# Performance work log

Measured on AMD Instinct MI355X. Metric: run time of the kernel, lower is better.

## Reference

```python
import jax, jax.numpy as jnp
import numpy as np

NUM_HEADS = 8
CHUNK = 64


def _retention(q, k, v):
    # q, k: (B, H, L, DK); v: (B, H, L, DV). Chunked linear retention with
    # per-head exponential decay gamma_h = 1 - 2^(-5-h) (RetNet convention).
    B, Hn, L, DK = q.shape
    DV = v.shape[-1]
    C = CHUNK
    N = L // C
    dt = q.dtype
    gamma = (1.0 - jnp.exp2(-5.0 - jnp.arange(Hn, dtype=jnp.float32))).astype(dt)  # (H,)
    q = q * (DK ** -0.5)
    idx = jnp.arange(C)
    diff = idx[:, None] - idx[None, :]
    # intra-chunk causal decay mask D[h,i,j] = gamma_h^(i-j) for i>=j else 0
    D = jnp.where(diff >= 0, gamma[:, None, None] ** diff, 0.0).astype(dt)      # (H,C,C)
    decay_q = (gamma[:, None] ** (idx[None, :] + 1)).astype(dt)                 # (H,C)
    decay_k = (gamma[:, None] ** (C - 1 - idx[None, :])).astype(dt)             # (H,C)
    decay_s = (gamma ** C).astype(dt)                                           # (H,)

    def to_chunks(x):
        return jnp.moveaxis(x.reshape(B, Hn, N, C, -1), 2, 0)  # (N,B,H,C,d)

    qs, ks, vs = map(to_chunks, (q, k, v))

    def step(S, x):
        qc, kc, vc = x  # (B,H,C,dk) / (B,H,C,dv)
        attn = jnp.einsum('bhid,bhjd->bhij', qc, kc) * D
        o_intra = jnp.einsum('bhij,bhje->bhie', attn, vc)
        o_inter = jnp.einsum('bhid,bhde->bhie', qc * decay_q[None, :, :, None], S)
        S_new = decay_s[None, :, None, None] * S + jnp.einsum(
            'bhjd,bhje->bhde', kc * decay_k[None, :, :, None], vc)
        return S_new, o_intra + o_inter

    S0 = jnp.zeros((B, Hn, DK, DV), dt)
    _, o = jax.lax.scan(step, S0, (qs, ks, vs))  # (N,B,H,C,DV)
    return jnp.moveaxis(o, 0, 2).reshape(B, Hn, L, DV)


def _xavier(key, fan_in, fan_out, gain=2 ** (-2.5)):
    limit = gain * np.sqrt(6.0 / (fan_in + fan_out))
    return jax.random.uniform(key, (fan_in, fan_out), jnp.float32, -limit, limit)


def setup_inputs() -> dict:
    key = jax.random.key(0)
    k0, k1, k2, k3, k4 = jax.random.split(key, 5)
    B, L, D = 2, 4096, 1024
    return {
        'hidden_states': jax.random.normal(k0, (B, L, D), jnp.float32),
        'rel_pos': jnp.zeros((1,), jnp.float32),  # unused by the module's forward
        'Wq': _xavier(k1, D, D),
        'Wk': _xavier(k2, D, D),
        'Wv': _xavier(k3, D, D),
        'Wo': _xavier(k4, D, D),
    }


def reference(hidden_states, rel_pos, Wq, Wk, Wv, Wo):
    B, L, Dm = hidden_states.shape
    Hd = Dm // NUM_HEADS
    q = (hidden_states @ Wq).reshape(B, L, NUM_HEADS, Hd).transpose(0, 2, 1, 3)
    k = (hidden_states @ Wk).reshape(B, L, NUM_HEADS, Hd).transpose(0, 2, 1, 3)
    v = (hidden_states @ Wv).reshape(B, L, NUM_HEADS, Hd).transpose(0, 2, 1, 3)
    o = _retention(q, k, v)  # (B,H,L,Hd)
    o = o.transpose(0, 2, 1, 3).reshape(B, L, Dm)
    return o @ Wo
```

## Files before the change

kernel.cpp:

```cpp
#include <hip/hip_runtime.h>
#include <hip/hip_bf16.h>

typedef __bf16 bf16;
typedef __bf16 bf16x8 __attribute__((ext_vector_type(8)));
typedef float f32x4 __attribute__((ext_vector_type(4)));

#define MFMA16(a, b, c) __builtin_amdgcn_mfma_f32_16x16x32_bf16((a), (b), (c), 0, 0, 0)


__device__ __forceinline__ void g2l16(const bf16* g, bf16* l) {
  __builtin_amdgcn_global_load_lds(
      (const __attribute__((address_space(1))) void*)g,
      (__attribute__((address_space(3))) void*)l, 16, 0, 0);
}

__global__ __launch_bounds__(256) void cvt_bf16(const float* __restrict__ X,
                                                bf16* __restrict__ Y) {
  const size_t i = ((size_t)blockIdx.x * 256 + threadIdx.x) * 8;
  float4 a = *(const float4*)&X[i];
  float4 b = *(const float4*)&X[i + 4];
  union { bf16 h[8]; uint4 u; } p;
  p.h[0] = (bf16)a.x; p.h[1] = (bf16)a.y; p.h[2] = (bf16)a.z; p.h[3] = (bf16)a.w;
  p.h[4] = (bf16)b.x; p.h[5] = (bf16)b.y; p.h[6] = (bf16)b.z; p.h[7] = (bf16)b.w;
  *(uint4*)&Y[i] = p.u;
}

__global__ __launch_bounds__(256) void transpose_w(
    const float* __restrict__ Wq, const float* __restrict__ Wk,
    const float* __restrict__ Wv, const float* __restrict__ Wo,
    bf16* __restrict__ Wt) {
  __shared__ bf16 t[64 * 72];
  const float* src = (blockIdx.z == 0) ? Wq : (blockIdx.z == 1) ? Wk
                     : (blockIdx.z == 2) ? Wv : Wo;
  bf16* dst = Wt + (size_t)blockIdx.z * 1024 * 1024;
  const int k0 = blockIdx.x * 64, n0 = blockIdx.y * 64;
  const int tid = threadIdx.x;
#pragma unroll
  for (int s = 0; s < 4; ++s) {
    int u = tid + s * 256;
    int r = u >> 4, c4 = (u & 15) * 4;
    float4 f = *(const float4*)&src[(size_t)(k0 + r) * 1024 + n0 + c4];
    t[r * 72 + c4 + 0] = (bf16)f.x;
    t[r * 72 + c4 + 1] = (bf16)f.y;
    t[r * 72 + c4 + 2] = (bf16)f.z;
    t[r * 72 + c4 + 3] = (bf16)f.w;
  }
  __syncthreads();
#pragma unroll
  for (int s = 0; s < 2; ++s) {
    int u = tid + s * 256;
    int r = u >> 3, cc = u & 7;
    union { bf16 h[8]; uint4 u4; } pk;
#pragma unroll
    for (int j = 0; j < 8; ++j) pk.h[j] = t[(cc * 8 + j) * 72 + r];
    *(uint4*)&dst[(size_t)(n0 + r) * 1024 + k0 + cc * 8] = pk.u4;
  }
}

template <typename TC, int QKV>
__global__ __launch_bounds__(256) void gemm_lds(
    const bf16* __restrict__ A, const bf16* __restrict__ Bt,
    TC* __restrict__ C, float alpha) {
  __shared__ bf16 lA[128 * 64];
  __shared__ bf16 lB[128 * 64];
  const int m0 = blockIdx.x * 128, n0 = blockIdx.y * 128;
  if (QKV) {
    Bt += (size_t)blockIdx.z * 1024 * 1024;
    C += (size_t)blockIdx.z * 8192 * 1024;
    if (blockIdx.z != 0) alpha = 1.0f;
  }
  const int tid = threadIdx.x;
  const int w = tid >> 6, lane = tid & 63, lr = lane & 15, quad = lane >> 4;
  const int wm = w >> 1, wn = w & 1;

  const int srow = w * 32 + (lane >> 3);
  const int clog = (lane & 7) ^ ((lane >> 3) & 7);
  const bf16* gA = A + (size_t)(m0 + srow) * 1024 + clog * 8;
  const bf16* gB = Bt + (size_t)(n0 + srow) * 1024 + clog * 8;

  f32x4 acc[4][4] = {};

  for (int it = 0; it < 16; ++it) {
    const int k0 = it * 64;
#pragma unroll
    for (int is = 0; is < 4; ++is) {
      g2l16(gA + (size_t)is * 8 * 1024 + k0, &lA[(w * 32 + is * 8) * 64]);
      g2l16(gB + (size_t)is * 8 * 1024 + k0, &lB[(w * 32 + is * 8) * 64]);
    }
    __syncthreads();
#pragma unroll
    for (int kk = 0; kk < 2; ++kk) {
      bf16x8 af[4], bfv[4];
#pragma unroll
      for (int i = 0; i < 4; ++i) {
        const int m = wm * 64 + i * 16 + lr;
        af[i] = *(bf16x8*)&lA[m * 64 + (((kk * 4 + quad) ^ (lr & 7)) * 8)];
      }
#pragma unroll
      for (int j = 0; j < 4; ++j) {
        const int n = wn * 64 + j * 16 + lr;
        bfv[j] = *(bf16x8*)&lB[n * 64 + (((kk * 4 + quad) ^ (lr & 7)) * 8)];
      }
#pragma unroll
      for (int i = 0; i < 4; ++i)
#pragma unroll
        for (int j = 0; j < 4; ++j)
          acc[i][j] = MFMA16(af[i], bfv[j], acc[i][j]);
    }
    __syncthreads();
  }
#pragma unroll
  for (int i = 0; i < 4; ++i) {
#pragma unroll
    for (int j = 0; j < 4; ++j) {
      const int row = m0 + wm * 64 + i * 16 + quad * 4;
      const int col = n0 + wn * 64 + j * 16 + lr;
#pragma unroll
      for (int r = 0; r < 4; ++r)
        C[(size_t)(row + r) * 1024 + col] = (TC)(acc[i][j][r] * alpha);
    }
  }
}

__global__ __launch_bounds__(256) void chunk_kv(
    const bf16* __restrict__ kb, const bf16* __restrict__ vb,
    bf16* __restrict__ Tb) {
  __shared__ bf16 lK[128 * 72];
  __shared__ bf16 lV[128 * 72];
  const int g = blockIdx.x;
  const int bh = g >> 6, n = g & 63, b = bh >> 3, h = bh & 7;
  const float log2g = log2f(1.0f - exp2f(-5.0f - (float)h));
  const int tid = threadIdx.x;
  const size_t rowbase = (size_t)(b * 4096 + n * 64) * 1024 + h * 128;
  const bf16* kc = kb + rowbase;
  const bf16* vc = vb + rowbase;
#pragma unroll
  for (int s = 0; s < 4; ++s) {
    int u = tid + s * 256;
    int c = u >> 4, d0 = (u & 15) * 8;
    union { uint4 u4; bf16 h8[8]; } kv, vv;
    kv.u4 = *(const uint4*)&kc[(size_t)c * 1024 + d0];
    vv.u4 = *(const uint4*)&vc[(size_t)c * 1024 + d0];
    const float dec = exp2f((float)(63 - c) * log2g);
#pragma unroll
    for (int j = 0; j < 8; ++j) {
      lK[(d0 + j) * 72 + c] = (bf16)((float)kv.h8[j] * dec);
      lV[(d0 + j) * 72 + c] = vv.h8[j];
    }
  }
  __syncthreads();
  const int w = tid >> 6, lane = tid & 63, lr = lane & 15, quad = lane >> 4;
  const int wm = w >> 1, wn = w & 1;
  f32x4 acc[4][4] = {};
#pragma unroll
  for (int kk = 0; kk < 2; ++kk) {
    bf16x8 af[4], bv[4];
#pragma unroll
    for (int i = 0; i < 4; ++i)
      af[i] = *(bf16x8*)&lK[(wm * 64 + i * 16 + lr) * 72 + kk * 32 + quad * 8];
#pragma unroll
    for (int j = 0; j < 4; ++j)
      bv[j] = *(bf16x8*)&lV[(wn * 64 + j * 16 + lr) * 72 + kk * 32 + quad * 8];
#pragma unroll
    for (int i = 0; i < 4; ++i)
#pragma unroll
      for (int j = 0; j < 4; ++j)
        acc[i][j] = MFMA16(af[i], bv[j], acc[i][j]);
  }
  bf16* tchunk = Tb + (size_t)g * 16384;
#pragma unroll
  for (int i = 0; i < 4; ++i) {
#pragma unroll
    for (int j = 0; j < 4; ++j) {
      const int dk = wm * 64 + i * 16 + quad * 4;
      const int dv = wn * 64 + j * 16 + lr;
      union { bf16 h4[4]; uint2 u2; } pk;
#pragma unroll
      for (int r = 0; r < 4; ++r) pk.h4[r] = (bf16)acc[i][j][r];
      *(uint2*)&tchunk[(size_t)dv * 128 + dk] = pk.u2;
    }
  }
}

__global__ __launch_bounds__(256) void scan_state(bf16* __restrict__ Tb) {
  const int blk = blockIdx.x;
  const int bh = blk >> 6, seg = blk & 63, h = bh & 7;
  const float gs = exp2f(64.0f * log2f(1.0f - exp2f(-5.0f - (float)h)));
  const size_t base = (size_t)bh * 64 * 16384 + (size_t)seg * 256 + threadIdx.x;
  float S = 0.0f;
#pragma unroll 8
  for (int n = 0; n < 64; ++n) {
    const size_t a = base + (size_t)n * 16384;
    const float t = (float)Tb[a];
    Tb[a] = (bf16)S;
    S = gs * S + t;
  }
}

__global__ __launch_bounds__(256) void chunk_out(
    const bf16* __restrict__ qb, const bf16* __restrict__ kb,
    const bf16* __restrict__ vb, const bf16* __restrict__ Sp,
    bf16* __restrict__ ob) {
  __shared__ bf16 lQ[64 * 136];
  __shared__ bf16 lK[64 * 136];
  __shared__ bf16 lVt[128 * 72];
  __shared__ bf16 lP[64 * 72];
  const int g = blockIdx.x;
  const int bh = g >> 6, n = g & 63, b = bh >> 3, h = bh & 7;
  const float log2g = log2f(1.0f - exp2f(-5.0f - (float)h));
  const int tid = threadIdx.x;
  const size_t rowbase = (size_t)(b * 4096 + n * 64) * 1024 + h * 128;
  const bf16* qc = qb + rowbase;
  const bf16* kc = kb + rowbase;
  const bf16* vc = vb + rowbase;
#pragma unroll
  for (int s = 0; s < 4; ++s) {
    int u = tid + s * 256;
    int c = u >> 4, d0 = (u & 15) * 8;
    *(uint4*)&lQ[c * 136 + d0] = *(const uint4*)&qc[(size_t)c * 1024 + d0];
    *(uint4*)&lK[c * 136 + d0] = *(const uint4*)&kc[(size_t)c * 1024 + d0];
    union { uint4 u4; bf16 h8[8]; } vv;
    vv.u4 = *(const uint4*)&vc[(size_t)c * 1024 + d0];
#pragma unroll
    for (int j = 0; j < 8; ++j) lVt[(d0 + j) * 72 + c] = vv.h8[j];
  }
  __syncthreads();
  const int w = tid >> 6, lane = tid & 63, lr = lane & 15, quad = lane >> 4;

  f32x4 p[4] = {};
#pragma unroll
  for (int kk = 0; kk < 4; ++kk) {
    bf16x8 bfrag = *(bf16x8*)&lK[(w * 16 + lr) * 136 + kk * 32 + quad * 8];
#pragma unroll
    for (int i = 0; i < 4; ++i) {
      bf16x8 afrag = *(bf16x8*)&lQ[(i * 16 + lr) * 136 + kk * 32 + quad * 8];
      p[i] = MFMA16(afrag, bfrag, p[i]);
    }
  }
#pragma unroll
  for (int i = 0; i < 4; ++i) {
#pragma unroll
    for (int r = 0; r < 4; ++r) {
      const int row = i * 16 + quad * 4 + r;
      const int col = w * 16 + lr;
      const int diff = row - col;
      const float val =
          (diff >= 0) ? p[i][r] * exp2f((float)diff * log2g) : 0.0f;
      lP[row * 72 + col] = (bf16)val;
    }
  }
  __syncthreads();

  f32x4 oacc[4][2] = {};
#pragma unroll
  for (int j = 0; j < 2; ++j) {
    const int dvt = w * 32 + j * 16;
#pragma unroll
    for (int kk = 0; kk < 2; ++kk) {
      bf16x8 bfrag = *(bf16x8*)&lVt[(dvt + lr) * 72 + kk * 32 + quad * 8];
#pragma unroll
      for (int i = 0; i < 4; ++i) {
        bf16x8 afrag = *(bf16x8*)&lP[(i * 16 + lr) * 72 + kk * 32 + quad * 8];
        oacc[i][j] = MFMA16(afrag, bfrag, oacc[i][j]);
      }
    }
  }

  const bf16* sp = Sp + (size_t)g * 16384;
#pragma unroll
  for (int kk = 0; kk < 4; ++kk) {
    bf16x8 aN[4];
#pragma unroll
    for (int i = 0; i < 4; ++i) {
      bf16x8 a0 = *(bf16x8*)&lQ[(i * 16 + lr) * 136 + kk * 32 + quad * 8];
      const float dq = exp2f((float)(i * 16 + lr + 1) * log2g);
#pragma unroll
      for (int e = 0; e < 8; ++e) a0[e] = (bf16)((float)a0[e] * dq);
      aN[i] = a0;
    }
#pragma unroll
    for (int j = 0; j < 2; ++j) {
      bf16x8 bfrag =
          *(const bf16x8*)&sp[(size_t)(w * 32 + j * 16 + lr) * 128 + kk * 32 + quad * 8];
#pragma unroll
      for (int i = 0; i < 4; ++i) oacc[i][j] = MFMA16(aN[i], bfrag, oacc[i][j]);
    }
  }

  bf16* oc = ob + rowbase;
#pragma unroll
  for (int i = 0; i < 4; ++i)
#pragma unroll
    for (int j = 0; j < 2; ++j)
#pragma unroll
      for (int r = 0; r < 4; ++r) {
        const int row = i * 16 + quad * 4 + r;
        const int col = w * 32 + j * 16 + lr;
        oc[(size_t)row * 1024 + col] = (bf16)oacc[i][j][r];
      }
}

extern "C" void kernel_launch(void* const* d_in, const int* in_sizes, int n_in,
                              void* d_out, int out_size, void* d_ws,
                              size_t ws_size, hipStream_t stream) {
  const float* X  = (const float*)d_in[0];
  const float* Wq = (const float*)d_in[2];
  const float* Wk = (const float*)d_in[3];
  const float* Wv = (const float*)d_in[4];
  const float* Wo = (const float*)d_in[5];

  char* ws = (char*)d_ws;
  const size_t SZ_QKV = (size_t)8192 * 1024 * sizeof(bf16);
  bf16* qb = (bf16*)(ws);
  bf16* ob = (bf16*)(ws + 3 * SZ_QKV);
  bf16* Tb = (bf16*)(ws + 4 * SZ_QKV);
  bf16* Wt = (bf16*)(ws + 6 * SZ_QKV);
  bf16* Xb = (bf16*)(ws + 6 * SZ_QKV + (size_t)4 * 1024 * 1024 * sizeof(bf16));
  bf16* kb = qb + (size_t)8192 * 1024;
  bf16* vb = kb + (size_t)8192 * 1024;

  cvt_bf16<<<4096, 256, 0, stream>>>(X, Xb);
  transpose_w<<<dim3(16, 16, 4), 256, 0, stream>>>(Wq, Wk, Wv, Wo, Wt);

  const float qscale = 0.08838834764831845f;
  gemm_lds<bf16, 1><<<dim3(64, 8, 3), 256, 0, stream>>>(Xb, Wt, qb, qscale);

  chunk_kv<<<1024, 256, 0, stream>>>(kb, vb, Tb);
  scan_state<<<1024, 256, 0, stream>>>(Tb);
  chunk_out<<<1024, 256, 0, stream>>>(qb, kb, vb, Tb, ob);

  gemm_lds<float, 0><<<dim3(64, 8), 256, 0, stream>>>(
      ob, Wt + (size_t)3 * 1024 * 1024, (float*)d_out, 1.0f);
}
```

Before: 232.4 us.

## Emit chunk-transposed K/V from QKV GEMM and streamline retention kernels

```diff
diff --git a/kernel.cpp b/kernel.cpp
--- a/kernel.cpp
+++ b/kernel.cpp
@@ -14,27 +14,30 @@
       (__attribute__((address_space(3))) void*)l, 16, 0, 0);
 }
 
-__global__ __launch_bounds__(256) void cvt_bf16(const float* __restrict__ X,
-                                                bf16* __restrict__ Y) {
-  const size_t i = ((size_t)blockIdx.x * 256 + threadIdx.x) * 8;
-  float4 a = *(const float4*)&X[i];
-  float4 b = *(const float4*)&X[i + 4];
-  union { bf16 h[8]; uint4 u; } p;
-  p.h[0] = (bf16)a.x; p.h[1] = (bf16)a.y; p.h[2] = (bf16)a.z; p.h[3] = (bf16)a.w;
-  p.h[4] = (bf16)b.x; p.h[5] = (bf16)b.y; p.h[6] = (bf16)b.z; p.h[7] = (bf16)b.w;
-  *(uint4*)&Y[i] = p.u;
-}
-
-__global__ __launch_bounds__(256) void transpose_w(
-    const float* __restrict__ Wq, const float* __restrict__ Wk,
-    const float* __restrict__ Wv, const float* __restrict__ Wo,
-    bf16* __restrict__ Wt) {
+__global__ __launch_bounds__(256) void prep(
+    const float* __restrict__ X, const float* __restrict__ Wq,
+    const float* __restrict__ Wk, const float* __restrict__ Wv,
+    const float* __restrict__ Wo, bf16* __restrict__ Wt,
+    bf16* __restrict__ Xb) {
+  const int tid = threadIdx.x;
+  if (blockIdx.z == 4) {
+#pragma unroll
+    for (int it = 0; it < 16; ++it) {
+      const size_t i = (((size_t)blockIdx.x * 16 + it) * 256 + tid) * 8;
+      float4 a = *(const float4*)&X[i];
+      float4 b = *(const float4*)&X[i + 4];
+      union { bf16 h[8]; uint4 u; } p;
+      p.h[0] = (bf16)a.x; p.h[1] = (bf16)a.y; p.h[2] = (bf16)a.z; p.h[3] = (bf16)a.w;
+      p.h[4] = (bf16)b.x; p.h[5] = (bf16)b.y; p.h[6] = (bf16)b.z; p.h[7] = (bf16)b.w;
+      *(uint4*)&Xb[i] = p.u;
+    }
+    return;
+  }
   __shared__ bf16 t[64 * 72];
   const float* src = (blockIdx.z == 0) ? Wq : (blockIdx.z == 1) ? Wk
                      : (blockIdx.z == 2) ? Wv : Wo;
   bf16* dst = Wt + (size_t)blockIdx.z * 1024 * 1024;
-  const int k0 = blockIdx.x * 64, n0 = blockIdx.y * 64;
-  const int tid = threadIdx.x;
+  const int k0 = (blockIdx.x >> 4) * 64, n0 = (blockIdx.x & 15) * 64;
 #pragma unroll
   for (int s = 0; s < 4; ++s) {
     int u = tid + s * 256;
@@ -57,16 +60,16 @@
   }
 }
 
-template <typename TC, int QKV>
+template <typename TC, int MODE>
 __global__ __launch_bounds__(256) void gemm_lds(
     const bf16* __restrict__ A, const bf16* __restrict__ Bt,
-    TC* __restrict__ C, float alpha) {
+    TC* __restrict__ C, bf16* __restrict__ kTb, bf16* __restrict__ vTb,
+    float alpha) {
   __shared__ bf16 lA[128 * 64];
   __shared__ bf16 lB[128 * 64];
   const int m0 = blockIdx.x * 128, n0 = blockIdx.y * 128;
-  if (QKV) {
+  if (MODE) {
     Bt += (size_t)blockIdx.z * 1024 * 1024;
-    C += (size_t)blockIdx.z * 8192 * 1024;
     if (blockIdx.z != 0) alpha = 1.0f;
   }
   const int tid = threadIdx.x;
@@ -115,38 +118,54 @@
     for (int j = 0; j < 4; ++j) {
       const int row = m0 + wm * 64 + i * 16 + quad * 4;
       const int col = n0 + wn * 64 + j * 16 + lr;
-#pragma unroll
-      for (int r = 0; r < 4; ++r)
-        C[(size_t)(row + r) * 1024 + col] = (TC)(acc[i][j][r] * alpha);
+      if (MODE == 0 || blockIdx.z < 2) {
+        TC* Cz = C + (MODE ? (size_t)blockIdx.z * 8192 * 1024 : 0);
+#pragma unroll
+        for (int r = 0; r < 4; ++r)
+          Cz[(size_t)(row + r) * 1024 + col] = (TC)(acc[i][j][r] * alpha);
+      }
+      if (MODE == 1 && blockIdx.z >= 1) {
+        bf16* Tp = (blockIdx.z == 1) ? kTb : vTb;
+        const int b = row >> 12, pos = row & 4095;
+        const int n = pos >> 6, c0 = pos & 63;
+        const int h = col >> 7, d = col & 127;
+        union { bf16 h4[4]; uint2 u2; } pk;
+#pragma unroll
+        for (int r = 0; r < 4; ++r) pk.h4[r] = (bf16)acc[i][j][r];
+        *(uint2*)&Tp[((size_t)((b * 8 + h) * 64 + n)) * 8192 + d * 64 + c0] = pk.u2;
+      }
     }
   }
 }
 
 __global__ __launch_bounds__(256) void chunk_kv(
-    const bf16* __restrict__ kb, const bf16* __restrict__ vb,
+    const bf16* __restrict__ kT, const bf16* __restrict__ vT,
     bf16* __restrict__ Tb) {
-  __shared__ bf16 lK[128 * 72];
-  __shared__ bf16 lV[128 * 72];
+  __shared__ bf16 lK[128 * 64];
+  __shared__ bf16 lV[128 * 64];
   const int g = blockIdx.x;
-  const int bh = g >> 6, n = g & 63, b = bh >> 3, h = bh & 7;
-  const float log2g = log2f(1.0f - exp2f(-5.0f - (float)h));
+  const int h = (g >> 6) & 7;
+  const float lg = log2f(1.0f - exp2f(-5.0f - (float)h));
+  const float ginv = exp2f(-lg);
   const int tid = threadIdx.x;
-  const size_t rowbase = (size_t)(b * 4096 + n * 64) * 1024 + h * 128;
-  const bf16* kc = kb + rowbase;
-  const bf16* vc = vb + rowbase;
+  const bf16* ks = kT + (size_t)g * 8192;
+  const bf16* vs = vT + (size_t)g * 8192;
 #pragma unroll
   for (int s = 0; s < 4; ++s) {
     int u = tid + s * 256;
-    int c = u >> 4, d0 = (u & 15) * 8;
-    union { uint4 u4; bf16 h8[8]; } kv, vv;
-    kv.u4 = *(const uint4*)&kc[(size_t)c * 1024 + d0];
-    vv.u4 = *(const uint4*)&vc[(size_t)c * 1024 + d0];
-    const float dec = exp2f((float)(63 - c) * log2g);
-#pragma unroll
-    for (int j = 0; j < 8; ++j) {
-      lK[(d0 + j) * 72 + c] = (bf16)((float)kv.h8[j] * dec);
-      lV[(d0 + j) * 72 + c] = vv.h8[j];
-    }
+    int d = u >> 3, c0 = (u & 7) * 8;
+    int pc = ((u & 7) ^ (d & 7)) * 8;
+    *(uint4*)&lV[d * 64 + pc] = *(const uint4*)&vs[d * 64 + c0];
+    union { uint4 u4; bf16 h8[8]; } kv;
+    kv.u4 = *(const uint4*)&ks[d * 64 + c0];
+    float e = exp2f((float)(63 - c0) * lg);
+    union { bf16 h8[8]; uint4 u4; } o;
+#pragma unroll
+    for (int jj = 0; jj < 8; ++jj) {
+      o.h8[jj] = (bf16)((float)kv.h8[jj] * e);
+      e *= ginv;
+    }
+    *(uint4*)&lK[d * 64 + pc] = o.u4;
   }
   __syncthreads();
   const int w = tid >> 6, lane = tid & 63, lr = lane & 15, quad = lane >> 4;
@@ -154,13 +173,14 @@
   f32x4 acc[4][4] = {};
 #pragma unroll
   for (int kk = 0; kk < 2; ++kk) {
+    const int pc = ((kk * 4 + quad) ^ (lr & 7)) * 8;
     bf16x8 af[4], bv[4];
 #pragma unroll
     for (int i = 0; i < 4; ++i)
-      af[i] = *(bf16x8*)&lK[(wm * 64 + i * 16 + lr) * 72 + kk * 32 + quad * 8];
+      af[i] = *(bf16x8*)&lK[(wm * 64 + i * 16 + lr) * 64 + pc];
 #pragma unroll
     for (int j = 0; j < 4; ++j)
-      bv[j] = *(bf16x8*)&lV[(wn * 64 + j * 16 + lr) * 72 + kk * 32 + quad * 8];
+      bv[j] = *(bf16x8*)&lV[(wn * 64 + j * 16 + lr) * 64 + pc];
 #pragma unroll
     for (int i = 0; i < 4; ++i)
 #pragma unroll
@@ -184,45 +204,50 @@
 
 __global__ __launch_bounds__(256) void scan_state(bf16* __restrict__ Tb) {
   const int blk = blockIdx.x;
-  const int bh = blk >> 6, seg = blk & 63, h = bh & 7;
+  const int bh = blk >> 4, h = bh & 7;
   const float gs = exp2f(64.0f * log2f(1.0f - exp2f(-5.0f - (float)h)));
-  const size_t base = (size_t)bh * 64 * 16384 + (size_t)seg * 256 + threadIdx.x;
-  float S = 0.0f;
+  const size_t base =
+      (size_t)bh * 1048576 + (size_t)(blk & 15) * 1024 + threadIdx.x * 4;
+  float S0 = 0.0f, S1 = 0.0f, S2 = 0.0f, S3 = 0.0f;
 #pragma unroll 8
   for (int n = 0; n < 64; ++n) {
     const size_t a = base + (size_t)n * 16384;
-    const float t = (float)Tb[a];
-    Tb[a] = (bf16)S;
-    S = gs * S + t;
+    union { uint2 u; bf16 h4[4]; } t, o;
+    t.u = *(const uint2*)&Tb[a];
+    o.h4[0] = (bf16)S0; o.h4[1] = (bf16)S1;
+    o.h4[2] = (bf16)S2; o.h4[3] = (bf16)S3;
+    *(uint2*)&Tb[a] = o.u;
+    S0 = gs * S0 + (float)t.h4[0];
+    S1 = gs * S1 + (float)t.h4[1];
+    S2 = gs * S2 + (float)t.h4[2];
+    S3 = gs * S3 + (float)t.h4[3];
   }
 }
 
 __global__ __launch_bounds__(256) void chunk_out(
     const bf16* __restrict__ qb, const bf16* __restrict__ kb,
-    const bf16* __restrict__ vb, const bf16* __restrict__ Sp,
+    const bf16* __restrict__ vT, const bf16* __restrict__ Sp,
     bf16* __restrict__ ob) {
   __shared__ bf16 lQ[64 * 136];
-  __shared__ bf16 lK[64 * 136];
-  __shared__ bf16 lVt[128 * 72];
+  __shared__ bf16 lVt[128 * 64];
   __shared__ bf16 lP[64 * 72];
   const int g = blockIdx.x;
   const int bh = g >> 6, n = g & 63, b = bh >> 3, h = bh & 7;
-  const float log2g = log2f(1.0f - exp2f(-5.0f - (float)h));
+  const float lg = log2f(1.0f - exp2f(-5.0f - (float)h));
+  const float gam = exp2f(lg);
   const int tid = threadIdx.x;
   const size_t rowbase = (size_t)(b * 4096 + n * 64) * 1024 + h * 128;
   const bf16* qc = qb + rowbase;
   const bf16* kc = kb + rowbase;
-  const bf16* vc = vb + rowbase;
+  const bf16* vs = vT + (size_t)g * 8192;
 #pragma unroll
   for (int s = 0; s < 4; ++s) {
     int u = tid + s * 256;
     int c = u >> 4, d0 = (u & 15) * 8;
     *(uint4*)&lQ[c * 136 + d0] = *(const uint4*)&qc[(size_t)c * 1024 + d0];
-    *(uint4*)&lK[c * 136 + d0] = *(const uint4*)&kc[(size_t)c * 1024 + d0];
-    union { uint4 u4; bf16 h8[8]; } vv;
-    vv.u4 = *(const uint4*)&vc[(size_t)c * 1024 + d0];
-#pragma unroll
-    for (int j = 0; j < 8; ++j) lVt[(d0 + j) * 72 + c] = vv.h8[j];
+    int d = u >> 3, cc = (u & 7) * 8;
+    int pc = ((u & 7) ^ (d & 7)) * 8;
+    *(uint4*)&lVt[d * 64 + pc] = *(const uint4*)&vs[d * 64 + cc];
   }
   __syncthreads();
   const int w = tid >> 6, lane = tid & 63, lr = lane & 15, quad = lane >> 4;
@@ -230,7 +255,8 @@
   f32x4 p[4] = {};
 #pragma unroll
   for (int kk = 0; kk < 4; ++kk) {
-    bf16x8 bfrag = *(bf16x8*)&lK[(w * 16 + lr) * 136 + kk * 32 + quad * 8];
+    bf16x8 bfrag =
+        *(const bf16x8*)&kc[(size_t)(w * 16 + lr) * 1024 + kk * 32 + quad * 8];
 #pragma unroll
     for (int i = 0; i < 4; ++i) {
       bf16x8 afrag = *(bf16x8*)&lQ[(i * 16 + lr) * 136 + kk * 32 + quad * 8];
@@ -244,60 +270,58 @@
       const int row = i * 16 + quad * 4 + r;
       const int col = w * 16 + lr;
       const int diff = row - col;
-      const float val =
-          (diff >= 0) ? p[i][r] * exp2f((float)diff * log2g) : 0.0f;
+      const float val = (diff >= 0) ? p[i][r] * exp2f((float)diff * lg) : 0.0f;
       lP[row * 72 + col] = (bf16)val;
     }
   }
   __syncthreads();
 
-  f32x4 oacc[4][2] = {};
+  f32x4 oac[4][2] = {}, oin[4][2] = {};
 #pragma unroll
   for (int j = 0; j < 2; ++j) {
-    const int dvt = w * 32 + j * 16;
 #pragma unroll
     for (int kk = 0; kk < 2; ++kk) {
-      bf16x8 bfrag = *(bf16x8*)&lVt[(dvt + lr) * 72 + kk * 32 + quad * 8];
+      const int m = w * 32 + j * 16 + lr;
+      bf16x8 bfrag = *(bf16x8*)&lVt[m * 64 + (((kk * 4 + quad) ^ (m & 7)) * 8)];
 #pragma unroll
       for (int i = 0; i < 4; ++i) {
         bf16x8 afrag = *(bf16x8*)&lP[(i * 16 + lr) * 72 + kk * 32 + quad * 8];
-        oacc[i][j] = MFMA16(afrag, bfrag, oacc[i][j]);
-      }
-    }
-  }
-
+        oac[i][j] = MFMA16(afrag, bfrag, oac[i][j]);
+      }
+    }
+  }
   const bf16* sp = Sp + (size_t)g * 16384;
 #pragma unroll
   for (int kk = 0; kk < 4; ++kk) {
-    bf16x8 aN[4];
-#pragma unroll
-    for (int i = 0; i < 4; ++i) {
-      bf16x8 a0 = *(bf16x8*)&lQ[(i * 16 + lr) * 136 + kk * 32 + quad * 8];
-      const float dq = exp2f((float)(i * 16 + lr + 1) * log2g);
-#pragma unroll
-      for (int e = 0; e < 8; ++e) a0[e] = (bf16)((float)a0[e] * dq);
-      aN[i] = a0;
-    }
+    bf16x8 af[4];
+#pragma unroll
+    for (int i = 0; i < 4; ++i)
+      af[i] = *(bf16x8*)&lQ[(i * 16 + lr) * 136 + kk * 32 + quad * 8];
 #pragma unroll
     for (int j = 0; j < 2; ++j) {
       bf16x8 bfrag =
           *(const bf16x8*)&sp[(size_t)(w * 32 + j * 16 + lr) * 128 + kk * 32 + quad * 8];
 #pragma unroll
-      for (int i = 0; i < 4; ++i) oacc[i][j] = MFMA16(aN[i], bfrag, oacc[i][j]);
+      for (int i = 0; i < 4; ++i) oin[i][j] = MFMA16(af[i], bfrag, oin[i][j]);
     }
   }
 
   bf16* oc = ob + rowbase;
 #pragma unroll
-  for (int i = 0; i < 4; ++i)
-#pragma unroll
-    for (int j = 0; j < 2; ++j)
+  for (int i = 0; i < 4; ++i) {
+    const float d0 = exp2f((float)(i * 16 + quad * 4 + 1) * lg);
+#pragma unroll
+    for (int j = 0; j < 2; ++j) {
+      float d = d0;
 #pragma unroll
       for (int r = 0; r < 4; ++r) {
         const int row = i * 16 + quad * 4 + r;
         const int col = w * 32 + j * 16 + lr;
-        oc[(size_t)row * 1024 + col] = (bf16)oacc[i][j][r];
-      }
+        oc[(size_t)row * 1024 + col] = (bf16)(oac[i][j][r] + d * oin[i][j][r]);
+        d *= gam;
+      }
+    }
+  }
 }
 
 extern "C" void kernel_launch(void* const* d_in, const int* in_sizes, int n_in,
@@ -310,25 +334,26 @@
   const float* Wo = (const float*)d_in[5];
 
   char* ws = (char*)d_ws;
-  const size_t SZ_QKV = (size_t)8192 * 1024 * sizeof(bf16);
-  bf16* qb = (bf16*)(ws);
-  bf16* ob = (bf16*)(ws + 3 * SZ_QKV);
-  bf16* Tb = (bf16*)(ws + 4 * SZ_QKV);
-  bf16* Wt = (bf16*)(ws + 6 * SZ_QKV);
-  bf16* Xb = (bf16*)(ws + 6 * SZ_QKV + (size_t)4 * 1024 * 1024 * sizeof(bf16));
-  bf16* kb = qb + (size_t)8192 * 1024;
-  bf16* vb = kb + (size_t)8192 * 1024;
-
-  cvt_bf16<<<4096, 256, 0, stream>>>(X, Xb);
-  transpose_w<<<dim3(16, 16, 4), 256, 0, stream>>>(Wq, Wk, Wv, Wo, Wt);
+  const size_t MB = 1024 * 1024;
+  bf16* qb  = (bf16*)(ws);
+  bf16* kb  = (bf16*)(ws + 16 * MB);
+  bf16* kTb = (bf16*)(ws + 32 * MB);
+  bf16* vTb = (bf16*)(ws + 48 * MB);
+  bf16* Tb  = (bf16*)(ws + 64 * MB);
+  bf16* Wt  = (bf16*)(ws + 96 * MB);
+  bf16* Xb  = (bf16*)(ws + 104 * MB);
+  bf16* ob  = Xb;
+
+  prep<<<dim3(256, 1, 5), 256, 0, stream>>>(X, Wq, Wk, Wv, Wo, Wt, Xb);
 
   const float qscale = 0.08838834764831845f;
-  gemm_lds<bf16, 1><<<dim3(64, 8, 3), 256, 0, stream>>>(Xb, Wt, qb, qscale);
-
-  chunk_kv<<<1024, 256, 0, stream>>>(kb, vb, Tb);
-  scan_state<<<1024, 256, 0, stream>>>(Tb);
-  chunk_out<<<1024, 256, 0, stream>>>(qb, kb, vb, Tb, ob);
+  gemm_lds<bf16, 1><<<dim3(64, 8, 3), 256, 0, stream>>>(Xb, Wt, qb, kTb, vTb,
+                                                        qscale);
+
+  chunk_kv<<<1024, 256, 0, stream>>>(kTb, vTb, Tb);
+  scan_state<<<256, 256, 0, stream>>>(Tb);
+  chunk_out<<<1024, 256, 0, stream>>>(qb, kb, vTb, Tb, ob);
 
   gemm_lds<float, 0><<<dim3(64, 8), 256, 0, stream>>>(
-      ob, Wt + (size_t)3 * 1024 * 1024, (float*)d_out, 1.0f);
-}
+      ob, Wt + (size_t)3 * 1024 * 1024, (float*)d_out, nullptr, nullptr, 1.0f);
+}
```

Measured after the change: 232.6 us. Within noise of the previous version (+0.1%).
